# Kernel optimization log

Measured on AMD Instinct MI355X. Metric: run time of the kernel, lower is better.

## Reference

```python
import jax, jax.numpy as jnp
import numpy as np


def _pairwise_dist(x, y):
    # x: [b, n, d], y: [b, n, d] -> squared L2 distances [b, n, n]
    xx = jnp.sum(x * x, axis=-1)  # [b, n]
    yy = jnp.sum(y * y, axis=-1)  # [b, n]
    zz = jnp.einsum('bnd,bmd->bnm', x, y)  # [b, n, n]
    return xx[:, :, None] + yy[:, None, :] - 2.0 * zz


def setup_inputs() -> dict:
    key = jax.random.key(0)
    k1, k2 = jax.random.split(key)
    bs, n, d = 4, 8192, 3
    x = jax.random.normal(k1, (bs, n, d), dtype=jnp.float32)
    y = jax.random.normal(k2, (bs, n, d), dtype=jnp.float32)
    return {"x": x, "y": y}


def reference(x, y):
    bs, n_points, _ = x.shape
    dist1 = jnp.sqrt(_pairwise_dist(x, y))  # [b, n, n]
    values1 = jnp.min(dist1, axis=2)        # [b, n] min over y for each x point
    dist2 = jnp.sqrt(_pairwise_dist(y, x))
    values2 = jnp.min(dist2, axis=2)        # min over x for each y point
    a = jnp.sum(values1, axis=1) / n_points
    b = jnp.sum(values2, axis=1) / n_points
    return jnp.sum(a) / bs + jnp.sum(b) / bs
```

## Files before the change

kernel.cpp:

```cpp
#include <hip/hip_runtime.h>
#include <stdint.h>

typedef _Float16 half8 __attribute__((ext_vector_type(8)));
typedef float f32x16 __attribute__((ext_vector_type(16)));

#define NPTS 8192
#define BS 4
#define TOTQ 65536
#define TPB 256
#define NS 4
#define QPB 512
#define NCHUNK 4

#define AS1 __attribute__((address_space(1)))
#define AS3 __attribute__((address_space(3)))

__device__ __forceinline__ float4 f4min(float4 a, float4 b) {
    return make_float4(fminf(a.x, b.x), fminf(a.y, b.y), fminf(a.z, b.z), fminf(a.w, b.w));
}


__global__ __launch_bounds__(TPB) void pack_mfma_kernel(const float* __restrict__ x,
                                                        const float* __restrict__ y,
                                                        ushort* __restrict__ Afrag,
                                                        ushort* __restrict__ Bfrag,
                                                        float* __restrict__ nq) {
    int pid = blockIdx.x * TPB + threadIdx.x;
    const float* src = (pid < BS * NPTS) ? x : y;
    int idx = pid & (BS * NPTS - 1);
    float p0 = src[idx * 3 + 0], p1 = src[idx * 3 + 1], p2 = src[idx * 3 + 2];
    float nt = p0 * p0 + p1 * p1 + p2 * p2;

    _Float16 h0 = (_Float16)p0, h1 = (_Float16)p1, h2 = (_Float16)p2;
    _Float16 l0 = (_Float16)(p0 - (float)h0);
    _Float16 l1 = (_Float16)(p1 - (float)h1);
    _Float16 l2 = (_Float16)(p2 - (float)h2);
    _Float16 nh = (_Float16)nt;
    _Float16 nl = (_Float16)(nt - (float)nh);
    _Float16 t2 = (_Float16)-2.0f;
    _Float16 m0 = t2 * h0, m1 = t2 * h1, m2 = t2 * h2;
    _Float16 n0 = t2 * l0, n1 = t2 * l1, n2 = t2 * l2;
    _Float16 one = (_Float16)1.0f, zz = (_Float16)0.0f;

    half8 ag0 = {m0, m1, m2, n0, n1, n2, m0, m1};
    half8 ag1 = {m2, one, one, n0, n1, n2, zz, zz};
    half8 bg0 = {h0, h1, h2, h0, h1, h2, l0, l1};
    half8 bg1 = {l2, nh, nl, l0, l1, l2, zz, zz};

    int qid = pid;
    int tid2 = pid ^ (BS * NPTS);
    size_t ab = (size_t)(qid >> 5) * 512 + (size_t)(qid & 31) * 8;
    *(half8*)(Afrag + ab)       = ag0;
    *(half8*)(Afrag + ab + 256) = ag1;
    size_t bb = (size_t)(tid2 >> 5) * 512 + (size_t)(tid2 & 31) * 8;
    *(half8*)(Bfrag + bb)       = bg0;
    *(half8*)(Bfrag + bb + 256) = bg1;
    nq[qid] = nt;
}

__global__ __launch_bounds__(TPB, 2) void mfma_min_kernel(const ushort* __restrict__ Afrag,
                                                          const ushort* __restrict__ Bfrag,
                                                          float* __restrict__ partial) {
    __shared__ __align__(16) char lds[2][16384];
    const int tid = threadIdx.x;
    const int wave = tid >> 6;
    const int l = tid & 63;
    const int chunkid = blockIdx.x / NS;
    const int s = blockIdx.x % NS;
    const int qbase = chunkid * QPB;
    const int dir = qbase >> 15;
    const int b = (qbase >> 13) & 3;
    const int tbase = dir * (BS * NPTS) + b * NPTS + s * (NPTS / NS);

    half8 afr0, afr1, afr2, afr3;
    {
        const ushort* Aw = Afrag + ((size_t)(qbase >> 5) + wave * 4) * 512 + (size_t)l * 8;
        afr0 = *(const half8*)(Aw);
        afr1 = *(const half8*)(Aw + 512);
        afr2 = *(const half8*)(Aw + 1024);
        afr3 = *(const half8*)(Aw + 1536);
    }
    f32x16 mrun0, mrun1, mrun2, mrun3, zc;
#pragma unroll
    for (int r = 0; r < 16; ++r) {
        mrun0[r] = 3.4e38f; mrun1[r] = 3.4e38f;
        mrun2[r] = 3.4e38f; mrun3[r] = 3.4e38f;
        zc[r] = 0.0f;
    }

    const char* gB = (const char*)Bfrag + (size_t)(tbase >> 5) * 1024;

#define STAGE(buf, c)                                                                       \
    {                                                                                       \
        _Pragma("unroll")                                                                   \
        for (int i = 0; i < 4; ++i)                                                         \
            __builtin_amdgcn_global_load_lds(                                               \
                (const AS1 uint32_t*)(gB + (size_t)(c) * 16384 + i * 4096 + tid * 16),      \
                (AS3 uint32_t*)(&lds[buf][i * 4096 + wave * 1024]), 16, 0, 0);              \
    }

#define AGROUP(AF, MR, BB0, BB1)                                                            \
    {                                                                                       \
        f32x16 d0 = __builtin_amdgcn_mfma_f32_32x32x16_f16(AF, BB0, zc, 0, 0, 0);           \
        f32x16 d1 = __builtin_amdgcn_mfma_f32_32x32x16_f16(AF, BB1, zc, 0, 0, 0);           \
        _Pragma("unroll")                                                                   \
        for (int r = 0; r < 16; ++r)                                                        \
            MR[r] = fminf(fminf(MR[r], d0[r]), d1[r]);                          \
    }

#define COMPUTE(BB0, BB1)                                                                   \
    AGROUP(afr0, mrun0, BB0, BB1)                                                           \
    AGROUP(afr1, mrun1, BB0, BB1)                                                           \
    AGROUP(afr2, mrun2, BB0, BB1)                                                           \
    AGROUP(afr3, mrun3, BB0, BB1)

    STAGE(0, 0);
    __syncthreads();

    int cur = 0;
#pragma unroll 1
    for (int c = 0; c < NCHUNK; ++c) {
        if (c + 1 < NCHUNK) STAGE(cur ^ 1, c + 1);
        const char* B = lds[cur];
        half8 bA0 = *(const half8*)(B + l * 16);
        half8 bA1 = *(const half8*)(B + 1024 + l * 16);
        half8 bB0, bB1;
#pragma unroll 1
        for (int p = 0; p < 8; p += 2) {
            bB0 = *(const half8*)(B + (p + 1) * 2048 + l * 16);
            bB1 = *(const half8*)(B + (p + 1) * 2048 + 1024 + l * 16);
            COMPUTE(bA0, bA1);
            int pn = (p + 2) & 7;
            bA0 = *(const half8*)(B + pn * 2048 + l * 16);
            bA1 = *(const half8*)(B + pn * 2048 + 1024 + l * 16);
            COMPUTE(bB0, bB1);
        }
        if (c + 1 < NCHUNK) {
            __syncthreads();
            cur ^= 1;
        }
    }
#undef STAGE
#undef COMPUTE
#undef AGROUP

    __syncthreads();
    float* ep = (float*)(&lds[0][0]);
    const int hi4 = (l >> 5) * 4;
    const int col = l & 31;

#define EPASS(AA, MR)                                                                       \
    {                                                                                       \
        _Pragma("unroll")                                                                   \
        for (int r = 0; r < 16; ++r) {                                                      \
            int row = (r & 3) + 8 * (r >> 2) + hi4;                                         \
            ep[wave * 1152 + row * 36 + col] = MR[r];                                       \
        }                                                                                   \
    }                                                                                       \
    __syncthreads();                                                                        \
    if (tid < 128) {                                                                        \
        const float4* rp = (const float4*)(ep + (tid >> 5) * 1152 + (tid & 31) * 36);       \
        float4 a01 = f4min(rp[0], rp[1]), a23 = f4min(rp[2], rp[3]);                        \
        float4 a45 = f4min(rp[4], rp[5]), a67 = f4min(rp[6], rp[7]);                        \
        float4 t = f4min(f4min(a01, a23), f4min(a45, a67));                                 \
        float m = fminf(fminf(t.x, t.y), fminf(t.z, t.w));                                  \
        partial[(size_t)s * TOTQ + qbase + (tid >> 5) * 128 + (AA) * 32 + (tid & 31)] = m;  \
    }                                                                                       \
    __syncthreads();

    EPASS(0, mrun0)
    EPASS(1, mrun1)
    EPASS(2, mrun2)
    EPASS(3, mrun3)
#undef EPASS
}

__global__ __launch_bounds__(TPB) void combine_mfma_kernel(const float* __restrict__ partial,
                                                           const float* __restrict__ nq,
                                                           float* __restrict__ bsum) {
    int q = blockIdx.x * TPB + threadIdx.x;
    float m = partial[q];
#pragma unroll
    for (int s = 1; s < NS; ++s)
        m = fminf(m, partial[(size_t)s * TOTQ + q]);
    float d = sqrtf(fmaxf(m + nq[q], 0.0f));
    __shared__ float red[TPB];
    red[threadIdx.x] = d;
    __syncthreads();
    for (int off = TPB / 2; off > 0; off >>= 1) {
        if (threadIdx.x < off) red[threadIdx.x] += red[threadIdx.x + off];
        __syncthreads();
    }
    if (threadIdx.x == 0) bsum[blockIdx.x] = red[0];
}

__global__ __launch_bounds__(TPB) void final_kernel(const float* __restrict__ bsum,
                                                    float* __restrict__ out) {
    __shared__ float red[TPB];
    red[threadIdx.x] = bsum[threadIdx.x];
    __syncthreads();
    for (int off = TPB / 2; off > 0; off >>= 1) {
        if (threadIdx.x < off) red[threadIdx.x] += red[threadIdx.x + off];
        __syncthreads();
    }
    if (threadIdx.x == 0) out[0] = red[0] * (1.0f / 32768.0f);
}

#define QPT 8
#define QPBF (TPB * QPT)
#define NGROUP (TOTQ / QPBF)
#define FNS 8

__global__ __launch_bounds__(TPB) void pack_kernel(const float* __restrict__ x,
                                                   const float* __restrict__ y,
                                                   float4* __restrict__ px,
                                                   float4* __restrict__ py) {
    int i = blockIdx.x * TPB + threadIdx.x;
    if (i < BS * NPTS) {
        float x0 = x[i * 3 + 0], x1 = x[i * 3 + 1], x2 = x[i * 3 + 2];
        px[i] = make_float4(x0, x1, x2, x0 * x0 + x1 * x1 + x2 * x2);
        float y0 = y[i * 3 + 0], y1 = y[i * 3 + 1], y2 = y[i * 3 + 2];
        py[i] = make_float4(y0, y1, y2, y0 * y0 + y1 * y1 + y2 * y2);
    }
}

__global__ __launch_bounds__(TPB) void chamfer_min_kernel(const float4* __restrict__ px,
                                                          const float4* __restrict__ py,
                                                          float* __restrict__ partial) {
    constexpr int SLICE = NPTS / FNS;
    __shared__ float4 tile[SLICE];
    const int t = threadIdx.x;
    const int g = blockIdx.x / FNS;
    const int s = blockIdx.x % FNS;
    const int dir = g >> 4;
    const int b = (g >> 2) & 3;
    const int chunk = g & 3;
    const float4* q  = (dir == 0 ? px : py) + b * NPTS + chunk * QPBF;
    const float4* tg = (dir == 0 ? py : px) + b * NPTS + s * SLICE;
    float a0[QPT], a1[QPT], a2[QPT], qq[QPT], mv[QPT];
#pragma unroll
    for (int i = 0; i < QPT; ++i) {
        float4 v = q[i * TPB + t];
        a0[i] = -2.0f * v.x; a1[i] = -2.0f * v.y; a2[i] = -2.0f * v.z;
        qq[i] = v.w; mv[i] = 3.4e38f;
    }
#pragma unroll
    for (int i = 0; i < SLICE / TPB; ++i)
        tile[i * TPB + t] = tg[i * TPB + t];
    __syncthreads();
#pragma unroll 2
    for (int j = 0; j < SLICE; j += 2) {
        float4 v0 = tile[j], v1 = tile[j + 1];
#pragma unroll
        for (int i = 0; i < QPT; ++i) {
            float d0 = fmaf(a2[i], v0.z, fmaf(a1[i], v0.y, fmaf(a0[i], v0.x, v0.w)));
            float d1 = fmaf(a2[i], v1.z, fmaf(a1[i], v1.y, fmaf(a0[i], v1.x, v1.w)));
            mv[i] = fminf(fminf(mv[i], d0), d1);
        }
    }
    const int qg0 = g * QPBF;
#pragma unroll
    for (int i = 0; i < QPT; ++i)
        partial[(size_t)s * TOTQ + qg0 + i * TPB + t] = mv[i] + qq[i];
}

__global__ __launch_bounds__(TPB) void combine_kernel(const float* __restrict__ partial,
                                                      float* __restrict__ bsum) {
    int idx = blockIdx.x * TPB + threadIdx.x;
    float m = 3.4e38f;
#pragma unroll
    for (int s = 0; s < FNS; ++s)
        m = fminf(m, partial[(size_t)s * TOTQ + idx]);
    float d = sqrtf(fmaxf(m, 0.0f));
    __shared__ float red[TPB];
    red[threadIdx.x] = d;
    __syncthreads();
    for (int off = TPB / 2; off > 0; off >>= 1) {
        if (threadIdx.x < off) red[threadIdx.x] += red[threadIdx.x + off];
        __syncthreads();
    }
    if (threadIdx.x == 0) bsum[blockIdx.x] = red[0];
}

extern "C" void kernel_launch(void* const* d_in, const int* in_sizes, int n_in,
                              void* d_out, int out_size, void* d_ws, size_t ws_size,
                              hipStream_t stream) {
    const float* x = (const float*)d_in[0];
    const float* y = (const float*)d_in[1];
    float* out = (float*)d_out;
    char* ws = (char*)d_ws;

    const size_t off_B = 2ull << 20;
    const size_t off_nq = 4ull << 20;
    const size_t off_pt = off_nq + (size_t)TOTQ * 4;
    const size_t off_bs = off_pt + (size_t)NS * TOTQ * 4;
    const size_t need = off_bs + 1024;

    if (ws_size >= need) {
        ushort* Afrag = (ushort*)ws;
        ushort* Bfrag = (ushort*)(ws + off_B);
        float* nq = (float*)(ws + off_nq);
        float* partial = (float*)(ws + off_pt);
        float* bsum = (float*)(ws + off_bs);
        hipLaunchKernelGGL(pack_mfma_kernel, dim3(TOTQ / TPB), dim3(TPB), 0, stream,
                           x, y, Afrag, Bfrag, nq);
        hipLaunchKernelGGL(mfma_min_kernel, dim3((TOTQ / QPB) * NS), dim3(TPB), 0, stream,
                           Afrag, Bfrag, partial);
        hipLaunchKernelGGL(combine_mfma_kernel, dim3(TOTQ / TPB), dim3(TPB), 0, stream,
                           partial, nq, bsum);
        hipLaunchKernelGGL(final_kernel, dim3(1), dim3(TPB), 0, stream, bsum, out);
    } else {
        float4* px = (float4*)ws;
        float4* py = (float4*)(ws + 512 * 1024);
        float* partial = (float*)(ws + 1024 * 1024);
        float* bsum = (float*)(ws + 1024 * 1024 + (size_t)FNS * TOTQ * 4);
        hipLaunchKernelGGL(pack_kernel, dim3((BS * NPTS + TPB - 1) / TPB), dim3(TPB), 0, stream,
                           x, y, px, py);
        hipLaunchKernelGGL(chamfer_min_kernel, dim3(NGROUP * FNS), dim3(TPB), 0, stream,
                           px, py, partial);
        hipLaunchKernelGGL(combine_kernel, dim3(TOTQ / TPB), dim3(TPB), 0, stream,
                           partial, bsum);
        hipLaunchKernelGGL(final_kernel, dim3(1), dim3(TPB), 0, stream, bsum, out);
    }
}
```

Before: 33.81 us.

## Fuse fp16 fragment packing into MFMA min kernel and drop pack launch

Removes the separate pack kernel and builds the split-fp16 A and B MFMA fragments on the fly inside the min kernel. Raw xyz floats are loaded from global memory, converted into registers and written to LDS while the previous chunk computes. The combine kernel now recomputes the squared norms from the raw inputs. This saves one launch and the global round trip of the fragment buffers, but adds conversion work and register-staged loads in place of the direct global-to-LDS loads.

```diff
diff --git a/kernel.cpp b/kernel.cpp
--- a/kernel.cpp
+++ b/kernel.cpp
@@ -11,55 +11,42 @@
 #define NS 4
 #define QPB 512
 #define NCHUNK 4
-
-#define AS1 __attribute__((address_space(1)))
-#define AS3 __attribute__((address_space(3)))
+#define SLICE (NPTS / NS)
 
 __device__ __forceinline__ float4 f4min(float4 a, float4 b) {
     return make_float4(fminf(a.x, b.x), fminf(a.y, b.y), fminf(a.z, b.z), fminf(a.w, b.w));
 }
 
-
-__global__ __launch_bounds__(TPB) void pack_mfma_kernel(const float* __restrict__ x,
-                                                        const float* __restrict__ y,
-                                                        ushort* __restrict__ Afrag,
-                                                        ushort* __restrict__ Bfrag,
-                                                        float* __restrict__ nq) {
-    int pid = blockIdx.x * TPB + threadIdx.x;
-    const float* src = (pid < BS * NPTS) ? x : y;
-    int idx = pid & (BS * NPTS - 1);
-    float p0 = src[idx * 3 + 0], p1 = src[idx * 3 + 1], p2 = src[idx * 3 + 2];
+__device__ __forceinline__ void mk_afrag(float p0, float p1, float p2,
+                                         half8* ag0, half8* ag1) {
+    _Float16 h0 = (_Float16)p0, h1 = (_Float16)p1, h2 = (_Float16)p2;
+    _Float16 l0 = (_Float16)(p0 - (float)h0);
+    _Float16 l1 = (_Float16)(p1 - (float)h1);
+    _Float16 l2 = (_Float16)(p2 - (float)h2);
+    _Float16 t2 = (_Float16)-2.0f;
+    _Float16 m0 = t2 * h0, m1 = t2 * h1, m2 = t2 * h2;
+    _Float16 n0 = t2 * l0, n1 = t2 * l1, n2 = t2 * l2;
+    _Float16 one = (_Float16)1.0f, zz = (_Float16)0.0f;
+    *ag0 = (half8){m0, m1, m2, n0, n1, n2, m0, m1};
+    *ag1 = (half8){m2, one, one, n0, n1, n2, zz, zz};
+}
+
+__device__ __forceinline__ void mk_bfrag(float p0, float p1, float p2,
+                                         half8* bg0, half8* bg1) {
     float nt = p0 * p0 + p1 * p1 + p2 * p2;
-
     _Float16 h0 = (_Float16)p0, h1 = (_Float16)p1, h2 = (_Float16)p2;
     _Float16 l0 = (_Float16)(p0 - (float)h0);
     _Float16 l1 = (_Float16)(p1 - (float)h1);
     _Float16 l2 = (_Float16)(p2 - (float)h2);
     _Float16 nh = (_Float16)nt;
     _Float16 nl = (_Float16)(nt - (float)nh);
-    _Float16 t2 = (_Float16)-2.0f;
-    _Float16 m0 = t2 * h0, m1 = t2 * h1, m2 = t2 * h2;
-    _Float16 n0 = t2 * l0, n1 = t2 * l1, n2 = t2 * l2;
-    _Float16 one = (_Float16)1.0f, zz = (_Float16)0.0f;
-
-    half8 ag0 = {m0, m1, m2, n0, n1, n2, m0, m1};
-    half8 ag1 = {m2, one, one, n0, n1, n2, zz, zz};
-    half8 bg0 = {h0, h1, h2, h0, h1, h2, l0, l1};
-    half8 bg1 = {l2, nh, nl, l0, l1, l2, zz, zz};
-
-    int qid = pid;
-    int tid2 = pid ^ (BS * NPTS);
-    size_t ab = (size_t)(qid >> 5) * 512 + (size_t)(qid & 31) * 8;
-    *(half8*)(Afrag + ab)       = ag0;
-    *(half8*)(Afrag + ab + 256) = ag1;
-    size_t bb = (size_t)(tid2 >> 5) * 512 + (size_t)(tid2 & 31) * 8;
-    *(half8*)(Bfrag + bb)       = bg0;
-    *(half8*)(Bfrag + bb + 256) = bg1;
-    nq[qid] = nt;
-}
-
-__global__ __launch_bounds__(TPB, 2) void mfma_min_kernel(const ushort* __restrict__ Afrag,
-                                                          const ushort* __restrict__ Bfrag,
+    _Float16 zz = (_Float16)0.0f;
+    *bg0 = (half8){h0, h1, h2, h0, h1, h2, l0, l1};
+    *bg1 = (half8){l2, nh, nl, l0, l1, l2, zz, zz};
+}
+
+__global__ __launch_bounds__(TPB, 2) void mfma_min_kernel(const float* __restrict__ x,
+                                                          const float* __restrict__ y,
                                                           float* __restrict__ partial) {
     __shared__ __align__(16) char lds[2][16384];
     const int tid = threadIdx.x;
@@ -70,16 +57,25 @@
     const int qbase = chunkid * QPB;
     const int dir = qbase >> 15;
     const int b = (qbase >> 13) & 3;
-    const int tbase = dir * (BS * NPTS) + b * NPTS + s * (NPTS / NS);
+    const int qpt = qbase & (BS * NPTS - 1);
+    const int tpt = b * NPTS + s * SLICE;
+    const float* qsrc = (dir == 0) ? x : y;
+    const float* tsrc = (dir == 0) ? y : x;
 
     half8 afr0, afr1, afr2, afr3;
     {
-        const ushort* Aw = Afrag + ((size_t)(qbase >> 5) + wave * 4) * 512 + (size_t)l * 8;
-        afr0 = *(const half8*)(Aw);
-        afr1 = *(const half8*)(Aw + 512);
-        afr2 = *(const half8*)(Aw + 1024);
-        afr3 = *(const half8*)(Aw + 1536);
-    }
+        const int row = l & 31;
+#define MKA(AF, a)                                                                          \
+        {                                                                                   \
+            const float* p = qsrc + (size_t)(qpt + (wave * 4 + (a)) * 32 + row) * 3;        \
+            half8 g0, g1;                                                                   \
+            mk_afrag(p[0], p[1], p[2], &g0, &g1);                                           \
+            AF = (l < 32) ? g0 : g1;                                                        \
+        }
+        MKA(afr0, 0) MKA(afr1, 1) MKA(afr2, 2) MKA(afr3, 3)
+#undef MKA
+    }
+
     f32x16 mrun0, mrun1, mrun2, mrun3, zc;
 #pragma unroll
     for (int r = 0; r < 16; ++r) {
@@ -88,15 +84,24 @@
         zc[r] = 0.0f;
     }
 
-    const char* gB = (const char*)Bfrag + (size_t)(tbase >> 5) * 1024;
-
-#define STAGE(buf, c)                                                                       \
+    float2 rA, rB, rC;
+#define BLOAD(c)                                                                            \
     {                                                                                       \
-        _Pragma("unroll")                                                                   \
-        for (int i = 0; i < 4; ++i)                                                         \
-            __builtin_amdgcn_global_load_lds(                                               \
-                (const AS1 uint32_t*)(gB + (size_t)(c) * 16384 + i * 4096 + tid * 16),      \
-                (AS3 uint32_t*)(&lds[buf][i * 4096 + wave * 1024]), 16, 0, 0);              \
+        const float2* p = (const float2*)(tsrc + (size_t)(tpt + (c) * 512 + tid * 2) * 3);  \
+        rA = p[0]; rB = p[1]; rC = p[2];                                                    \
+    }
+#define BPACK(buf)                                                                          \
+    {                                                                                       \
+        const int t0 = tid * 2;                                                             \
+        const int base = (t0 >> 5) * 1024;                                                  \
+        const int r0 = (t0 & 31) * 16;                                                      \
+        half8 g0, g1;                                                                       \
+        mk_bfrag(rA.x, rA.y, rB.x, &g0, &g1);                                               \
+        *(half8*)(&lds[buf][base + r0]) = g0;                                               \
+        *(half8*)(&lds[buf][base + 512 + r0]) = g1;                                         \
+        mk_bfrag(rB.y, rC.x, rC.y, &g0, &g1);                                               \
+        *(half8*)(&lds[buf][base + r0 + 16]) = g0;                                          \
+        *(half8*)(&lds[buf][base + 512 + r0 + 16]) = g1;                                    \
     }
 
 #define AGROUP(AF, MR, BB0, BB1)                                                            \
@@ -114,13 +119,14 @@
     AGROUP(afr2, mrun2, BB0, BB1)                                                           \
     AGROUP(afr3, mrun3, BB0, BB1)
 
-    STAGE(0, 0);
+    BLOAD(0)
+    BPACK(0)
     __syncthreads();
 
     int cur = 0;
 #pragma unroll 1
     for (int c = 0; c < NCHUNK; ++c) {
-        if (c + 1 < NCHUNK) STAGE(cur ^ 1, c + 1);
+        if (c + 1 < NCHUNK) BLOAD(c + 1)
         const char* B = lds[cur];
         half8 bA0 = *(const half8*)(B + l * 16);
         half8 bA1 = *(const half8*)(B + 1024 + l * 16);
@@ -136,11 +142,13 @@
             COMPUTE(bB0, bB1);
         }
         if (c + 1 < NCHUNK) {
+            BPACK(cur ^ 1)
             __syncthreads();
             cur ^= 1;
         }
     }
-#undef STAGE
+#undef BLOAD
+#undef BPACK
 #undef COMPUTE
 #undef AGROUP
 
@@ -176,14 +184,21 @@
 }
 
 __global__ __launch_bounds__(TPB) void combine_mfma_kernel(const float* __restrict__ partial,
-                                                           const float* __restrict__ nq,
+                                                           const float* __restrict__ x,
+                                                           const float* __restrict__ y,
                                                            float* __restrict__ bsum) {
     int q = blockIdx.x * TPB + threadIdx.x;
+    int dir = q >> 15;
+    int pidx = q & (BS * NPTS - 1);
+    const float* src = (dir == 0) ? x : y;
+    float p0 = src[pidx * 3 + 0], p1 = src[pidx * 3 + 1], p2 = src[pidx * 3 + 2];
+    float nq = p0 * p0 + p1 * p1 + p2 * p2;
+
     float m = partial[q];
 #pragma unroll
     for (int s = 1; s < NS; ++s)
         m = fminf(m, partial[(size_t)s * TOTQ + q]);
-    float d = sqrtf(fmaxf(m + nq[q], 0.0f));
+    float d = sqrtf(fmaxf(m + nq, 0.0f));
     __shared__ float red[TPB];
     red[threadIdx.x] = d;
     __syncthreads();
@@ -227,8 +242,8 @@
 __global__ __launch_bounds__(TPB) void chamfer_min_kernel(const float4* __restrict__ px,
                                                           const float4* __restrict__ py,
                                                           float* __restrict__ partial) {
-    constexpr int SLICE = NPTS / FNS;
-    __shared__ float4 tile[SLICE];
+    constexpr int SLICEF = NPTS / FNS;
+    __shared__ float4 tile[SLICEF];
     const int t = threadIdx.x;
     const int g = blockIdx.x / FNS;
     const int s = blockIdx.x % FNS;
@@ -236,7 +251,7 @@
     const int b = (g >> 2) & 3;
     const int chunk = g & 3;
     const float4* q  = (dir == 0 ? px : py) + b * NPTS + chunk * QPBF;
-    const float4* tg = (dir == 0 ? py : px) + b * NPTS + s * SLICE;
+    const float4* tg = (dir == 0 ? py : px) + b * NPTS + s * SLICEF;
     float a0[QPT], a1[QPT], a2[QPT], qq[QPT], mv[QPT];
 #pragma unroll
     for (int i = 0; i < QPT; ++i) {
@@ -245,11 +260,11 @@
         qq[i] = v.w; mv[i] = 3.4e38f;
     }
 #pragma unroll
-    for (int i = 0; i < SLICE / TPB; ++i)
+    for (int i = 0; i < SLICEF / TPB; ++i)
         tile[i * TPB + t] = tg[i * TPB + t];
     __syncthreads();
 #pragma unroll 2
-    for (int j = 0; j < SLICE; j += 2) {
+    for (int j = 0; j < SLICEF; j += 2) {
         float4 v0 = tile[j], v1 = tile[j + 1];
 #pragma unroll
         for (int i = 0; i < QPT; ++i) {
@@ -290,24 +305,16 @@
     float* out = (float*)d_out;
     char* ws = (char*)d_ws;
 
-    const size_t off_B = 2ull << 20;
-    const size_t off_nq = 4ull << 20;
-    const size_t off_pt = off_nq + (size_t)TOTQ * 4;
-    const size_t off_bs = off_pt + (size_t)NS * TOTQ * 4;
+    const size_t off_bs = (size_t)NS * TOTQ * 4;
     const size_t need = off_bs + 1024;
 
     if (ws_size >= need) {
-        ushort* Afrag = (ushort*)ws;
-        ushort* Bfrag = (ushort*)(ws + off_B);
-        float* nq = (float*)(ws + off_nq);
-        float* partial = (float*)(ws + off_pt);
+        float* partial = (float*)ws;
         float* bsum = (float*)(ws + off_bs);
-        hipLaunchKernelGGL(pack_mfma_kernel, dim3(TOTQ / TPB), dim3(TPB), 0, stream,
-                           x, y, Afrag, Bfrag, nq);
         hipLaunchKernelGGL(mfma_min_kernel, dim3((TOTQ / QPB) * NS), dim3(TPB), 0, stream,
-                           Afrag, Bfrag, partial);
+                           x, y, partial);
         hipLaunchKernelGGL(combine_mfma_kernel, dim3(TOTQ / TPB), dim3(TPB), 0, stream,
-                           partial, nq, bsum);
+                           partial, x, y, bsum);
         hipLaunchKernelGGL(final_kernel, dim3(1), dim3(TPB), 0, stream, bsum, out);
     } else {
         float4* px = (float4*)ws;
```

Result: faster. 29.00 us (median of 2 runs) (-14.2%).
